# Kernel optimization log

Measured on AMD Instinct MI355X. Metric: run time of the kernel, lower is better.

## Reference

```python
import jax, jax.numpy as jnp
import numpy as np

# shapes
B, S, D, V = 2, 2048, 1024, 32000
C = 8            # n_cycles
P = 256          # actual planes = min(n_planes_init, D // 2)
EPS = 1.1920929e-07  # torch RMSNorm default eps for float32 (finfo.eps)


def _rmsnorm(x, w):
    ms = jnp.mean(x * x, axis=-1, keepdims=True)
    return x * jax.lax.rsqrt(ms + EPS) * w


def setup_inputs() -> dict:
    key = jax.random.key(0)
    ks = jax.random.split(key, 10)
    tokens = jax.random.randint(ks[0], (B, S), 0, V, dtype=jnp.int32)
    embed_weight = jax.random.normal(ks[1], (V, D), dtype=jnp.float32) * 0.02
    lm_head_weight = jax.random.normal(ks[2], (V, D), dtype=jnp.float32) * 0.02
    out_norm_weight = jnp.ones((D,), dtype=jnp.float32)
    # per-cycle learned params (non-trivial values for numerics)
    angles = jax.random.normal(ks[3], (C, P), dtype=jnp.float32) * 0.1
    scales = 1.0 + jax.random.normal(ks[4], (C, D), dtype=jnp.float32) * 0.01
    shifts = jax.random.normal(ks[5], (C, D), dtype=jnp.float32) * 0.01
    norm_weights = 1.0 + jax.random.normal(ks[6], (C, D), dtype=jnp.float32) * 0.01
    mix_weight = jnp.array([0.1, 0.8, 0.1], dtype=jnp.float32)
    # plane pairs: per-cycle permutation of D, pi = perm[:P], pj = perm[P:2P]
    pi_list, pj_list = [], []
    for c in range(C):
        perm = jax.random.permutation(jax.random.fold_in(ks[7], c), D)
        pi_list.append(perm[:P])
        pj_list.append(perm[P:2 * P])
    pi_all = jnp.stack(pi_list).astype(jnp.int32)  # [C, P]
    pj_all = jnp.stack(pj_list).astype(jnp.int32)  # [C, P]
    return {
        "tokens": tokens,
        "embed_weight": embed_weight,
        "angles": angles,
        "scales": scales,
        "shifts": shifts,
        "norm_weights": norm_weights,
        "mix_weight": mix_weight,
        "out_norm_weight": out_norm_weight,
        "lm_head_weight": lm_head_weight,
        "pi_all": pi_all,
        "pj_all": pj_all,
    }


def reference(tokens, embed_weight, angles, scales, shifts, norm_weights,
              mix_weight, out_norm_weight, lm_head_weight, pi_all, pj_all):
    x = embed_weight[tokens].astype(jnp.float32)  # [B, S, D]
    n_cycles = angles.shape[0]
    for c in range(n_cycles):
        # temporal mix: shifted-left / self / shifted-right
        left = jnp.pad(x[:, :-1, :], ((0, 0), (1, 0), (0, 0)))
        right = jnp.pad(x[:, 1:, :], ((0, 0), (0, 1), (0, 0)))
        x = mix_weight[0] * left + mix_weight[1] * x + mix_weight[2] * right
        # Givens rotations on disjoint plane pairs (gather -> rotate -> scatter)
        pi, pj = pi_all[c], pj_all[c]
        cos_a = jnp.cos(angles[c])
        sin_a = jnp.sin(angles[c])
        xi = x[..., pi]  # [B, S, P]
        xj = x[..., pj]
        x_new = x.at[..., pi].set(xi * cos_a - xj * sin_a)
        x_new = x_new.at[..., pj].set(xi * sin_a + xj * cos_a)
        # scale/shift + SiLU, then RMSNorm residual update
        x_act = jax.nn.silu(x_new * scales[c] + shifts[c])
        x = x + _rmsnorm(x_act - x, norm_weights[c])
    x = _rmsnorm(x, out_norm_weight)
    return jnp.einsum("bsd,vd->bsv", x, lm_head_weight)  # [B, S, V]
```

## Files before the change

### kernel.cpp

```cpp
#include <hip/hip_runtime.h>

#define B_SZ   2
#define S_LEN  2048
#define D_DIM  1024
#define V_DIM  32000
#define NTOK   (B_SZ * S_LEN)
#define NCYC   8
#define NPLANES 256
#define EPS_F  1.1920929e-07f
#define NTILE  2000

typedef float  f32x4  __attribute__((ext_vector_type(4)));
typedef __bf16 bf16x8 __attribute__((ext_vector_type(8)));

__device__ __forceinline__ unsigned short f32_to_bf16(float f) {
    unsigned int u = __builtin_bit_cast(unsigned int, f);
    u += 0x7fffu + ((u >> 16) & 1u);
    return (unsigned short)(u >> 16);
}

__global__ __launch_bounds__(512, 2) void k_chain(
    const int* __restrict__ tokens, const float* __restrict__ table,
    const float* __restrict__ angles, const float* __restrict__ scales,
    const float* __restrict__ shifts, const float* __restrict__ normw,
    const float* __restrict__ mixw, const float* __restrict__ outnw,
    const int* __restrict__ pi_all, const int* __restrict__ pj_all,
    const float* __restrict__ lmhead,
    unsigned short* __restrict__ xbf, unsigned short* __restrict__ wbf)
{
    __shared__ float lx[32][D_DIM];
    const int blk = blockIdx.x, tid = threadIdx.x;
    const int wv = tid >> 6, ln = tid & 63;
    const int t0 = blk << 4;
    const int s0 = t0 & (S_LEN - 1);
    const int seqbase = t0 & ~(S_LEN - 1);
    const int r0 = wv << 2;

    const float mw0 = mixw[0], mw1 = mixw[1], mw2 = mixw[2];

    bool valid[4];
    #pragma unroll
    for (int i = 0; i < 4; ++i) {
        const int r = r0 + i;
        const int s = s0 - 8 + r;
        valid[i] = (s >= 0) && (s < S_LEN);
        float4 v0 = make_float4(0.f,0.f,0.f,0.f), v1 = v0, v2 = v0, v3 = v0;
        if (valid[i]) {
            const float* tr = table + (size_t)tokens[seqbase + s] * D_DIM;
            v0 = *(const float4*)(tr +   0 + ln * 4);
            v1 = *(const float4*)(tr + 256 + ln * 4);
            v2 = *(const float4*)(tr + 512 + ln * 4);
            v3 = *(const float4*)(tr + 768 + ln * 4);
        }
        *(float4*)&lx[r][  0 + ln * 4] = v0;
        *(float4*)&lx[r][256 + ln * 4] = v1;
        *(float4*)&lx[r][512 + ln * 4] = v2;
        *(float4*)&lx[r][768 + ln * 4] = v3;
    }
    __syncthreads();

    float4 mreg[4][4];

    for (int c = 0; c < NCYC; ++c) {
        float4 sc[4], sh[4], nw[4];
        #pragma unroll
        for (int q = 0; q < 4; ++q) {
            sc[q] = *(const float4*)(scales + c * D_DIM + q * 256 + ln * 4);
            sh[q] = *(const float4*)(shifts + c * D_DIM + q * 256 + ln * 4);
            nw[q] = *(const float4*)(normw  + c * D_DIM + q * 256 + ln * 4);
        }
        int ip[4], jp[4];
        float sa[4], ca[4];
        #pragma unroll
        for (int u = 0; u < 4; ++u) {
            ip[u] = pi_all[c * NPLANES + ln * 4 + u];
            jp[u] = pj_all[c * NPLANES + ln * 4 + u];
            sincosf(angles[c * NPLANES + ln * 4 + u], &sa[u], &ca[u]);
        }

        #pragma unroll
        for (int i = 0; i < 4; ++i) {
            const int r = r0 + i;
            if (r >= c + 1 && r < 31 - c && valid[i]) {
                #pragma unroll
                for (int q = 0; q < 4; ++q) {
                    const float4 a = *(const float4*)&lx[r - 1][q * 256 + ln * 4];
                    const float4 b = *(const float4*)&lx[r    ][q * 256 + ln * 4];
                    const float4 d = *(const float4*)&lx[r + 1][q * 256 + ln * 4];
                    mreg[i][q].x = mw0 * a.x + mw1 * b.x + mw2 * d.x;
                    mreg[i][q].y = mw0 * a.y + mw1 * b.y + mw2 * d.y;
                    mreg[i][q].z = mw0 * a.z + mw1 * b.z + mw2 * d.z;
                    mreg[i][q].w = mw0 * a.w + mw1 * b.w + mw2 * d.w;
                }
            }
        }
        __syncthreads();
        #pragma unroll
        for (int i = 0; i < 4; ++i) {
            const int r = r0 + i;
            if (r >= c + 1 && r < 31 - c && valid[i]) {
                #pragma unroll
                for (int q = 0; q < 4; ++q)
                    *(float4*)&lx[r][q * 256 + ln * 4] = mreg[i][q];
            }
        }
        #pragma unroll
        for (int i = 0; i < 4; ++i) {
            const int r = r0 + i;
            if (r >= c + 1 && r < 31 - c && valid[i]) {
                float xi[4], xj[4];
                #pragma unroll
                for (int u = 0; u < 4; ++u) { xi[u] = lx[r][ip[u]]; xj[u] = lx[r][jp[u]]; }
                #pragma unroll
                for (int u = 0; u < 4; ++u) {
                    lx[r][ip[u]] = xi[u] * ca[u] - xj[u] * sa[u];
                    lx[r][jp[u]] = xi[u] * sa[u] + xj[u] * ca[u];
                }
            }
        }
        #pragma unroll
        for (int i = 0; i < 4; ++i) {
            const int r = r0 + i;
            if (r >= c + 1 && r < 31 - c && valid[i]) {
                float4 rr[4];
                float sum = 0.f;
                #pragma unroll
                for (int q = 0; q < 4; ++q) {
                    const float4 xn = *(const float4*)&lx[r][q * 256 + ln * 4];
                    const float a0 = xn.x * sc[q].x + sh[q].x;
                    const float a1 = xn.y * sc[q].y + sh[q].y;
                    const float a2 = xn.z * sc[q].z + sh[q].z;
                    const float a3 = xn.w * sc[q].w + sh[q].w;
                    rr[q].x = a0 / (1.f + expf(-a0)) - mreg[i][q].x;
                    rr[q].y = a1 / (1.f + expf(-a1)) - mreg[i][q].y;
                    rr[q].z = a2 / (1.f + expf(-a2)) - mreg[i][q].z;
                    rr[q].w = a3 / (1.f + expf(-a3)) - mreg[i][q].w;
                    sum += rr[q].x * rr[q].x + rr[q].y * rr[q].y
                         + rr[q].z * rr[q].z + rr[q].w * rr[q].w;
                }
                #pragma unroll
                for (int off = 32; off > 0; off >>= 1)
                    sum += __shfl_xor(sum, off, 64);
                const float inv = rsqrtf(sum * (1.0f / D_DIM) + EPS_F);
                #pragma unroll
                for (int q = 0; q < 4; ++q) {
                    float4 o;
                    o.x = mreg[i][q].x + rr[q].x * inv * nw[q].x;
                    o.y = mreg[i][q].y + rr[q].y * inv * nw[q].y;
                    o.z = mreg[i][q].z + rr[q].z * inv * nw[q].z;
                    o.w = mreg[i][q].w + rr[q].w * inv * nw[q].w;
                    *(float4*)&lx[r][q * 256 + ln * 4] = o;
                }
            }
        }
        {
            const int end = (c + 1) * 1024000;
            for (int idx = c * 1024000 + blk * 512 + tid; idx < end; idx += 131072) {
                const float4 v = ((const float4*)lmhead)[idx];
                const ushort4 o = make_ushort4(f32_to_bf16(v.x), f32_to_bf16(v.y),
                                               f32_to_bf16(v.z), f32_to_bf16(v.w));
                ((ushort4*)wbf)[idx] = o;
            }
        }
        __syncthreads();
    }

    float4 ow[4];
    #pragma unroll
    for (int q = 0; q < 4; ++q)
        ow[q] = *(const float4*)(outnw + q * 256 + ln * 4);
    #pragma unroll
    for (int e = 0; e < 2; ++e) {
        const int r = 8 + wv + e * 8;
        float4 v[4];
        float sum = 0.f;
        #pragma unroll
        for (int q = 0; q < 4; ++q) {
            v[q] = *(const float4*)&lx[r][q * 256 + ln * 4];
            sum += v[q].x * v[q].x + v[q].y * v[q].y
                 + v[q].z * v[q].z + v[q].w * v[q].w;
        }
        #pragma unroll
        for (int off = 32; off > 0; off >>= 1)
            sum += __shfl_xor(sum, off, 64);
        const float inv = rsqrtf(sum * (1.0f / D_DIM) + EPS_F);
        unsigned short* xr = xbf + (size_t)(t0 + r - 8) * D_DIM;
        #pragma unroll
        for (int q = 0; q < 4; ++q) {
            const ushort4 o = make_ushort4(f32_to_bf16(v[q].x * inv * ow[q].x),
                                           f32_to_bf16(v[q].y * inv * ow[q].y),
                                           f32_to_bf16(v[q].z * inv * ow[q].z),
                                           f32_to_bf16(v[q].w * inv * ow[q].w));
            *(ushort4*)(xr + q * 256 + ln * 4) = o;
        }
    }
}

#define GLD_LDS(g, l)                                                          \
    __builtin_amdgcn_global_load_lds(                                          \
        (const __attribute__((address_space(1))) void*)(g),                    \
        (__attribute__((address_space(3))) void*)(l), 16, 0, 0)

#define STAGE_A(BUF, H, KT, P) do {                                            \
    GLD_LDS((P) + (size_t)(H) * 131072 + (size_t)(KT) * 64,                    \
            &lds[(BUF) * 32768 + (H) * 8192 + wave * 1024]);                   \
    GLD_LDS((P) + (size_t)(H) * 131072 + 8192 + (size_t)(KT) * 64,             \
            &lds[(BUF) * 32768 + (H) * 8192 + wave * 1024 + 512]);             \
} while (0)

#define STAGE_B(BUF, H, KT, P) do {                                            \
    GLD_LDS((P) + (size_t)(H) * 131072 + (size_t)(KT) * 64,                    \
            &lds[16384 + (BUF) * 32768 + (H) * 8192 + wave * 1024]);           \
    GLD_LDS((P) + (size_t)(H) * 131072 + 8192 + (size_t)(KT) * 64,             \
            &lds[16384 + (BUF) * 32768 + (H) * 8192 + wave * 1024 + 512]);     \
} while (0)

#define RD_A(BUF, MIB) do { _Pragma("unroll")                                  \
    for (int q_ = 0; q_ < 4; ++q_) {                                           \
        afr[q_][0] = *(const bf16x8*)&lds[(BUF) * 32768 + aoff + ((MIB) + q_) * 1024 + kx0]; \
        afr[q_][1] = *(const bf16x8*)&lds[(BUF) * 32768 + aoff + ((MIB) + q_) * 1024 + kx1]; \
    } } while (0)

#define RD_B(BUF, NIB, DST) do { _Pragma("unroll")                             \
    for (int n_ = 0; n_ < 2; ++n_) {                                           \
        DST[n_][0] = *(const bf16x8*)&lds[(BUF) * 32768 + boff + ((NIB) + n_) * 1024 + kx0]; \
        DST[n_][1] = *(const bf16x8*)&lds[(BUF) * 32768 + boff + ((NIB) + n_) * 1024 + kx1]; \
    } } while (0)

#define MFMA16(MIB, NIB, BF) do {                                              \
    __builtin_amdgcn_s_setprio(1);                                             \
    _Pragma("unroll") for (int m_ = 0; m_ < 4; ++m_)                           \
    _Pragma("unroll") for (int n_ = 0; n_ < 2; ++n_) {                         \
        acc[(MIB) + m_][(NIB) + n_] = __builtin_amdgcn_mfma_f32_16x16x32_bf16( \
            afr[m_][0], BF[n_][0], acc[(MIB) + m_][(NIB) + n_], 0, 0, 0);      \
        acc[(MIB) + m_][(NIB) + n_] = __builtin_amdgcn_mfma_f32_16x16x32_bf16( \
            afr[m_][1], BF[n_][1], acc[(MIB) + m_][(NIB) + n_], 0, 0, 0);      \
    }                                                                          \
    __builtin_amdgcn_s_setprio(0); } while (0)

#define PH_SYNC() do { __builtin_amdgcn_s_barrier();                           \
    asm volatile("s_waitcnt lgkmcnt(0)" ::: "memory"); } while (0)
#define PH_END() do { asm volatile("" ::: "memory");                           \
    __builtin_amdgcn_s_barrier(); } while (0)
#define VMCNT4() asm volatile("s_waitcnt vmcnt(4)" ::: "memory")

__global__ __launch_bounds__(512, 2) void k_gemm(
    const unsigned short* __restrict__ A,
    const unsigned short* __restrict__ Bw,
    float* __restrict__ C)
{
    __shared__ __align__(16) unsigned short lds[65536];
    const int tid = threadIdx.x;
    const int wave = tid >> 6, lane = tid & 63;
    const int wm = wave >> 2, wn = wave & 3;
    const int lr = lane & 15, kg = lane >> 4;

    const int xr  = (lane & 7) * 8;
    const int kx0 = (kg * 8) ^ xr;
    const int kx1 = (32 + kg * 8) ^ xr;
    const int aoff = (wm * 128 + lr) * 64;
    const int boff = 16384 + (wn * 64 + lr) * 64;

    const int srow = lane >> 3;
    const int scol = ((lane & 7) ^ srow) * 8;
    const int soff = (wave * 16 + srow) * 1024 + scol;

    const int xcd = blockIdx.x & 7;
    const int rr  = blockIdx.x >> 3;
    const int tbase = xcd * 250 + rr * 8;
    const int ntile_mine = (rr == 31) ? 2 : 8;

    int T  = tbase;
    int bm = T & 15, bn = T >> 4;
    const unsigned short* gA = A  + (size_t)(bm * 256) * 1024 + soff;
    const unsigned short* gB = Bw + (size_t)(bn * 256) * 1024 + soff;

    bf16x8 afr[4][2], b01[2][2], b23[2][2];

    STAGE_A(0, 0, 0, gA); STAGE_A(0, 1, 0, gA);
    STAGE_B(0, 0, 0, gB); STAGE_B(0, 1, 0, gB);
    STAGE_B(1, 0, 1, gB); STAGE_B(1, 1, 1, gB);
    VMCNT4();
    __builtin_amdgcn_s_barrier();

    for (int t = 0; t < ntile_mine; ++t) {
        const bool last = (t == ntile_mine - 1);
        const int Tn = last ? T : T + 1;
        const int bm2 = Tn & 15, bn2 = Tn >> 4;
        const unsigned short* gA2 = A  + (size_t)(bm2 * 256) * 1024 + soff;
        const unsigned short* gB2 = Bw + (size_t)(bn2 * 256) * 1024 + soff;

        f32x4 acc[8][4];
        #pragma unroll
        for (int i = 0; i < 8; ++i)
            #pragma unroll
            for (int j2 = 0; j2 < 4; ++j2) acc[i][j2] = (f32x4){0.f, 0.f, 0.f, 0.f};

        for (int j = 0; j < 8; ++j) {
            const unsigned short* sA = (j == 7) ? gA2 : gA;
            const unsigned short* sB = (j == 7) ? gB2 : gB;
            const int k1 = 2 * j + 1;
            const int k2 = (2 * j + 2) & 15;
            const int k3 = (2 * j + 3) & 15;

            RD_A(0, 0); RD_B(0, 0, b01);
            STAGE_A(1, 0, k1, gA);
            PH_SYNC(); MFMA16(0, 0, b01); PH_END();

            RD_B(0, 2, b23);
            STAGE_A(1, 1, k1, gA);
            PH_SYNC(); MFMA16(0, 2, b23); PH_END();

            RD_A(0, 4);
            STAGE_B(0, 0, k2, sB);
            PH_SYNC(); MFMA16(4, 2, b23); PH_END();

            STAGE_B(0, 1, k2, sB);
            VMCNT4();
            PH_SYNC(); MFMA16(4, 0, b01); PH_END();

            RD_A(1, 0); RD_B(1, 0, b01);
            STAGE_A(0, 0, k2, sA);
            PH_SYNC(); MFMA16(0, 0, b01); PH_END();

            RD_B(1, 2, b23);
            STAGE_A(0, 1, k2, sA);
            PH_SYNC(); MFMA16(0, 2, b23); PH_END();

            RD_A(1, 4);
            STAGE_B(1, 0, k3, sB);
            PH_SYNC(); MFMA16(4, 2, b23); PH_END();

            STAGE_B(1, 1, k3, sB);
            VMCNT4();
            PH_SYNC(); MFMA16(4, 0, b01); PH_END();
        }

        #pragma unroll
        for (int mi = 0; mi < 8; ++mi) {
            const size_t m0 = (size_t)(bm * 256 + wm * 128 + mi * 16 + kg * 4);
            #pragma unroll
            for (int ni = 0; ni < 4; ++ni) {
                const int n = bn * 256 + wn * 64 + ni * 16 + lr;
                float* cp = C + m0 * V_DIM + n;
                cp[0]                 = acc[mi][ni][0];
                cp[(size_t)V_DIM]     = acc[mi][ni][1];
                cp[(size_t)2 * V_DIM] = acc[mi][ni][2];
                cp[(size_t)3 * V_DIM] = acc[mi][ni][3];
            }
        }

        T = Tn; bm = bm2; bn = bn2; gA = gA2; gB = gB2;
    }
}

extern "C" void kernel_launch(void* const* d_in, const int* in_sizes, int n_in,
                              void* d_out, int out_size, void* d_ws, size_t ws_size,
                              hipStream_t stream)
{
    const int*   tokens = (const int*)  d_in[0];
    const float* embedw = (const float*)d_in[1];
    const float* angles = (const float*)d_in[2];
    const float* scales = (const float*)d_in[3];
    const float* shifts = (const float*)d_in[4];
    const float* normw  = (const float*)d_in[5];
    const float* mixw   = (const float*)d_in[6];
    const float* outnw  = (const float*)d_in[7];
    const float* lmhead = (const float*)d_in[8];
    const int*   pi_all = (const int*)  d_in[9];
    const int*   pj_all = (const int*)  d_in[10];
    float* out = (float*)d_out;

    unsigned short* xbf = (unsigned short*)d_ws;
    unsigned short* wbf = xbf + (size_t)NTOK * D_DIM;

    k_chain<<<NTOK / 16, 512, 0, stream>>>(tokens, embedw, angles, scales,
        shifts, normw, mixw, outnw, pi_all, pj_all, lmhead, xbf, wbf);

    k_gemm<<<256, 512, 0, stream>>>(xbf, wbf, out);
}
```

Before: 410.9 us.

## Double-buffer MFMA register fragments to overlap LDS reads with MFMA in GEMM

Splits the A and B fragment registers into two alternating sets so the LDS reads for the next phase are issued before the current phase's MFMAs, rather than waiting on lgkmcnt(0) first. The explicit lgkmcnt waits are dropped and each phase is bracketed only by plain barriers. The aim is to hide LDS read latency behind matrix instructions, at the cost of more VGPRs (occupancy is pinned by launch bounds of 512,2) and a prologue read hoisted before the tile loop. Correctness depends on compiler-inserted waits, since barrier ordering versus pending LDS reads is now implicit.

```diff
diff --git a/kernel.cpp b/kernel.cpp
--- a/kernel.cpp
+++ b/kernel.cpp
@@ -215,10 +215,10 @@
             &lds[16384 + (BUF) * 32768 + (H) * 8192 + wave * 1024 + 512]);     \
 } while (0)
 
-#define RD_A(BUF, MIB) do { _Pragma("unroll")                                  \
+#define RD_AF(BUF, MIB, DST) do { _Pragma("unroll")                            \
     for (int q_ = 0; q_ < 4; ++q_) {                                           \
-        afr[q_][0] = *(const bf16x8*)&lds[(BUF) * 32768 + aoff + ((MIB) + q_) * 1024 + kx0]; \
-        afr[q_][1] = *(const bf16x8*)&lds[(BUF) * 32768 + aoff + ((MIB) + q_) * 1024 + kx1]; \
+        DST[q_][0] = *(const bf16x8*)&lds[(BUF) * 32768 + aoff + ((MIB) + q_) * 1024 + kx0]; \
+        DST[q_][1] = *(const bf16x8*)&lds[(BUF) * 32768 + aoff + ((MIB) + q_) * 1024 + kx1]; \
     } } while (0)
 
 #define RD_B(BUF, NIB, DST) do { _Pragma("unroll")                             \
@@ -227,21 +227,18 @@
         DST[n_][1] = *(const bf16x8*)&lds[(BUF) * 32768 + boff + ((NIB) + n_) * 1024 + kx1]; \
     } } while (0)
 
-#define MFMA16(MIB, NIB, BF) do {                                              \
+#define MFMA16(MIB, NIB, AF, BF) do {                                          \
     __builtin_amdgcn_s_setprio(1);                                             \
     _Pragma("unroll") for (int m_ = 0; m_ < 4; ++m_)                           \
     _Pragma("unroll") for (int n_ = 0; n_ < 2; ++n_) {                         \
         acc[(MIB) + m_][(NIB) + n_] = __builtin_amdgcn_mfma_f32_16x16x32_bf16( \
-            afr[m_][0], BF[n_][0], acc[(MIB) + m_][(NIB) + n_], 0, 0, 0);      \
+            AF[m_][0], BF[n_][0], acc[(MIB) + m_][(NIB) + n_], 0, 0, 0);       \
         acc[(MIB) + m_][(NIB) + n_] = __builtin_amdgcn_mfma_f32_16x16x32_bf16( \
-            afr[m_][1], BF[n_][1], acc[(MIB) + m_][(NIB) + n_], 0, 0, 0);      \
+            AF[m_][1], BF[n_][1], acc[(MIB) + m_][(NIB) + n_], 0, 0, 0);       \
     }                                                                          \
     __builtin_amdgcn_s_setprio(0); } while (0)
 
-#define PH_SYNC() do { __builtin_amdgcn_s_barrier();                           \
-    asm volatile("s_waitcnt lgkmcnt(0)" ::: "memory"); } while (0)
-#define PH_END() do { asm volatile("" ::: "memory");                           \
-    __builtin_amdgcn_s_barrier(); } while (0)
+#define BAR() __builtin_amdgcn_s_barrier()
 #define VMCNT4() asm volatile("s_waitcnt vmcnt(4)" ::: "memory")
 
 __global__ __launch_bounds__(512, 2) void k_gemm(
@@ -275,13 +272,15 @@
     const unsigned short* gA = A  + (size_t)(bm * 256) * 1024 + soff;
     const unsigned short* gB = Bw + (size_t)(bn * 256) * 1024 + soff;
 
-    bf16x8 afr[4][2], b01[2][2], b23[2][2];
+    bf16x8 afA[4][2], afB[4][2];
+    bf16x8 b01A[2][2], b23A[2][2], b01B[2][2], b23B[2][2];
 
     STAGE_A(0, 0, 0, gA); STAGE_A(0, 1, 0, gA);
     STAGE_B(0, 0, 0, gB); STAGE_B(0, 1, 0, gB);
     STAGE_B(1, 0, 1, gB); STAGE_B(1, 1, 1, gB);
     VMCNT4();
-    __builtin_amdgcn_s_barrier();
+    BAR();
+    RD_AF(0, 0, afA); RD_B(0, 0, b01A);
 
     for (int t = 0; t < ntile_mine; ++t) {
         const bool last = (t == ntile_mine - 1);
@@ -303,37 +302,46 @@
             const int k2 = (2 * j + 2) & 15;
             const int k3 = (2 * j + 3) & 15;
 
-            RD_A(0, 0); RD_B(0, 0, b01);
             STAGE_A(1, 0, k1, gA);
-            PH_SYNC(); MFMA16(0, 0, b01); PH_END();
-
-            RD_B(0, 2, b23);
+            BAR();
+            RD_B(0, 2, b23A);
+            MFMA16(0, 0, afA, b01A);
+            BAR();
             STAGE_A(1, 1, k1, gA);
-            PH_SYNC(); MFMA16(0, 2, b23); PH_END();
-
-            RD_A(0, 4);
+            BAR();
+            RD_AF(0, 4, afB);
+            MFMA16(0, 2, afA, b23A);
+            BAR();
             STAGE_B(0, 0, k2, sB);
-            PH_SYNC(); MFMA16(4, 2, b23); PH_END();
-
+            BAR();
+            MFMA16(4, 2, afB, b23A);
+            BAR();
             STAGE_B(0, 1, k2, sB);
             VMCNT4();
-            PH_SYNC(); MFMA16(4, 0, b01); PH_END();
-
-            RD_A(1, 0); RD_B(1, 0, b01);
+            BAR();
+            RD_AF(1, 0, afA); RD_B(1, 0, b01B);
+            MFMA16(4, 0, afB, b01A);
+            BAR();
             STAGE_A(0, 0, k2, sA);
-            PH_SYNC(); MFMA16(0, 0, b01); PH_END();
-
-            RD_B(1, 2, b23);
+            BAR();
+            RD_B(1, 2, b23B);
+            MFMA16(0, 0, afA, b01B);
+            BAR();
             STAGE_A(0, 1, k2, sA);
-            PH_SYNC(); MFMA16(0, 2, b23); PH_END();
-
-            RD_A(1, 4);
+            BAR();
+            RD_AF(1, 4, afB);
+            MFMA16(0, 2, afA, b23B);
+            BAR();
             STAGE_B(1, 0, k3, sB);
-            PH_SYNC(); MFMA16(4, 2, b23); PH_END();
-
+            BAR();
+            MFMA16(4, 2, afB, b23B);
+            BAR();
             STAGE_B(1, 1, k3, sB);
             VMCNT4();
-            PH_SYNC(); MFMA16(4, 0, b01); PH_END();
+            BAR();
+            RD_AF(0, 0, afA); RD_B(0, 0, b01A);
+            MFMA16(4, 0, afB, b01B);
+            BAR();
         }
 
         #pragma unroll
```

Result: slower. 799.0 us (+94.4%).
